# Optimization experiments

Measured on AMD Instinct MI355X. Metric: run time of the kernel, lower is better.

The kernel has to match this reference:

```python
import jax, jax.numpy as jnp
import numpy as np

P, NT = 4, 524288
DZ = 1.0e-3     # z step (m)
DT = 0.01       # time step (ps)
GAMMA = 1.0e-3  # nonlinear coefficient
FR = 0.18       # Raman fraction
OMEGA0 = 1830.0 # carrier angular frequency (rad/ps), ~1030 nm


def setup_inputs() -> dict:
    key = jax.random.key(0)
    ks = jax.random.split(key, 7)
    A_re = jax.random.normal(ks[0], (P, NT), jnp.float32) * 0.5
    A_im = jax.random.normal(ks[1], (P, NT), jnp.float32) * 0.5
    S = jax.random.uniform(ks[2], (P, P, P, P), jnp.float32) * 0.1  # mode overlap tensor
    D_re = jax.random.normal(ks[3], (P, NT), jnp.float32) * 0.1
    D_im = jax.random.normal(ks[4], (P, NT), jnp.float32) * 0.01
    hrw_re = jax.random.normal(ks[5], (NT,), jnp.float32)
    hrw_im = jax.random.normal(ks[6], (NT,), jnp.float32)
    omega = (2.0 * np.pi * np.fft.fftfreq(NT, DT)).astype(np.float32)
    return {"A_re": A_re, "A_im": A_im, "S": S, "D_re": D_re, "D_im": D_im,
            "hrw_re": hrw_re, "hrw_im": hrw_im, "omega": jnp.asarray(omega), "nz": 10}


def _propagate(A0, S, D, hrw, omega, nz):
    # half-step linear (dispersion) phase, applied in the frequency domain
    lin = jnp.exp(0.5j * DZ * D)                       # (P, Nt)
    # self-steepening spectral prefactor  i*gamma*(1 + Omega/omega0)
    pref = (1j * GAMMA) * (1.0 + omega / OMEGA0)       # (Nt,)
    hrw_c = jnp.conj(hrw)                              # (Nt,)

    def nl(A):  # dA/dz from Kerr + Raman + self-steepening, A: (P, Nt) time domain
        S_kerr = jnp.einsum('pqrs,qt,rt,st->pt', S, A, A, jnp.conj(A))
        T = A[:, None, :] * jnp.conj(A)[None, :, :]    # (P, P, Nt)
        T_conv = jnp.fft.ifft(jnp.fft.fft(T, axis=-1) * hrw_c, axis=-1) * DT
        Vpl = jnp.einsum('pmrs,rst->pmt', S, T_conv)   # (P, P, Nt)
        S_raman = jnp.einsum('pmt,mt->pt', Vpl, A)     # (P, Nt)
        S_total = (1.0 - FR) * S_kerr + FR * S_raman
        return jnp.fft.fft(pref * jnp.fft.ifft(S_total, axis=-1), axis=-1)

    def step(carry, _):
        f, fw = carry
        fw = fw * lin
        f = jnp.fft.fft(fw, axis=-1)
        # RK4 for the nonlinear sub-step
        k1 = DZ * nl(f)
        k2 = DZ * nl(f + 0.5 * k1)
        k3 = DZ * nl(f + 0.5 * k2)
        k4 = DZ * nl(f + k3)
        f = f + (k1 + 2.0 * k2 + 2.0 * k3 + k4) / 6.0
        fw = jnp.fft.ifft(f, axis=-1) * lin
        return (f, fw), None

    fw0 = jnp.fft.ifft(A0, axis=-1)
    (f, fw), _ = jax.lax.scan(step, (A0, fw0), None, length=nz)
    return jnp.fft.fft(fw, axis=-1)


def reference(A_re, A_im, S, D_re, D_im, hrw_re, hrw_im, omega, nz):
    A = (A_re + 1j * A_im).astype(jnp.complex64)
    D = (D_re + 1j * D_im).astype(jnp.complex64)
    hrw = (hrw_re + 1j * hrw_im).astype(jnp.complex64)
    out = _propagate(A, S, D, hrw, omega, nz)          # (P, Nt) complex64
    return jnp.stack([out.real, out.imag])             # (2, P, Nt) float32
```

## Files before the change

kernel.cpp:

```cpp
#include <hip/hip_runtime.h>
#include <math.h>

#define NTOT (1 << 19)
#define NN1 512
#define NN2 1024
#define PM 4
#define NZ_STEPS 10

static const float DZv = 1.0e-3f;
static const float DTv = 0.01f;
static const float GAMMAv = 1.0e-3f;
static const float FRv = 0.18f;
static const float OMEGA0v = 1830.0f;

typedef float2 cplx;
__device__ inline cplx cmul(cplx a, cplx b) { return make_float2(a.x * b.x - a.y * b.y, a.x * b.y + a.y * b.x); }
__device__ inline cplx cadd(cplx a, cplx b) { return make_float2(a.x + b.x, a.y + b.y); }
__device__ inline cplx csub(cplx a, cplx b) { return make_float2(a.x - b.x, a.y - b.y); }
__device__ inline cplx cscale(cplx a, float s) { return make_float2(a.x * s, a.y * s); }
__device__ inline cplx conjc(cplx a) { return make_float2(a.x, -a.y); }
__device__ inline cplx expi_pi(float a, float sgn) {
    float s, c;
    sincospif(a, &s, &c);
    return make_float2(c, sgn * s);
}
__device__ inline int dig4rev10(int j) {
    return ((j & 3) << 8) | (((j >> 2) & 3) << 6) | (((j >> 4) & 3) << 4) | (((j >> 6) & 3) << 2) | ((j >> 8) & 3);
}
__device__ inline int b4rev8(int t) {
    return ((t & 3) << 6) | (((t >> 2) & 3) << 4) | (((t >> 4) & 3) << 2) | ((t >> 6) & 3);
}
__device__ inline int islot_512(int k1) { return ((k1 & 1) << 8) | b4rev8(k1 >> 1); }

#define SK(q) ((q) + ((q) >> 4))

__device__ inline void wfence() {
    asm volatile("" ::: "memory");
    __builtin_amdgcn_wave_barrier();
    asm volatile("" ::: "memory");
}

#define TW_SZ 596
#define TWOFF(L) ((L) == 4 ? 0 : (L) == 16 ? 4 : (L) == 64 ? 20 : 84)
#define TWR2 340
__device__ inline void init_tw(cplx* tw, int tid) {
    for (int idx = tid; idx < TW_SZ; idx += 256) {
        float a;
        if (idx < 4) a = (float)idx * (0.5f / 4.0f);
        else if (idx < 20) a = (float)(idx - 4) * (0.5f / 16.0f);
        else if (idx < 84) a = (float)(idx - 20) * (0.5f / 64.0f);
        else if (idx < 340) a = (float)(idx - 84) * (0.5f / 256.0f);
        else a = (float)(idx - 340) * (1.0f / 256.0f);
        float s, c;
        sincospif(a, &s, &c);
        tw[idx] = make_float2(c, s);
    }
}
__device__ inline cplx twget(const cplx* tw, int off, int b, float SGN) {
    cplx t = tw[off + b];
    return make_float2(t.x, SGN * t.y);
}

__device__ inline void r4dif_w(cplx& x0, cplx& x1, cplx& x2, cplx& x3, cplx w1, float SGN) {
    cplx t0 = cadd(x0, x2), t1 = cadd(x1, x3), t2 = csub(x0, x2), t3 = csub(x1, x3);
    cplx ct3 = make_float2(-SGN * t3.y, SGN * t3.x);
    cplx w2 = cmul(w1, w1), w3 = cmul(w2, w1);
    x0 = cadd(t0, t1);
    x1 = cmul(cadd(t2, ct3), w1);
    x2 = cmul(csub(t0, t1), w2);
    x3 = cmul(csub(t2, ct3), w3);
}
__device__ inline void r4dif0(cplx& x0, cplx& x1, cplx& x2, cplx& x3, float SGN) {
    cplx t0 = cadd(x0, x2), t1 = cadd(x1, x3), t2 = csub(x0, x2), t3 = csub(x1, x3);
    cplx ct3 = make_float2(-SGN * t3.y, SGN * t3.x);
    x0 = cadd(t0, t1); x1 = cadd(t2, ct3); x2 = csub(t0, t1); x3 = csub(t2, ct3);
}
__device__ inline void r4dit_w(cplx& x0, cplx& x1, cplx& x2, cplx& x3, cplx w1, float SGN) {
    cplx w2 = cmul(w1, w1), w3 = cmul(w2, w1);
    cplx z1 = cmul(x1, w1), z2 = cmul(x2, w2), z3 = cmul(x3, w3);
    cplx t0 = cadd(x0, z2), t1 = cadd(z1, z3), t2 = csub(x0, z2), t3 = csub(z1, z3);
    cplx ct3 = make_float2(-SGN * t3.y, SGN * t3.x);
    x0 = cadd(t0, t1); x1 = cadd(t2, ct3); x2 = csub(t0, t1); x3 = csub(t2, ct3);
}
__device__ inline void r4dit0(cplx& x0, cplx& x1, cplx& x2, cplx& x3, float SGN) {
    cplx t0 = cadd(x0, x2), t1 = cadd(x1, x3), t2 = csub(x0, x2), t3 = csub(x1, x3);
    cplx ct3 = make_float2(-SGN * t3.y, SGN * t3.x);
    x0 = cadd(t0, t1); x1 = cadd(t2, ct3); x2 = csub(t0, t1); x3 = csub(t2, ct3);
}

template <int ISGN>
__device__ inline void fft_j2n2(const cplx* gsrc, cplx* y, cplx* ld, const cplx* tw, int tid) {
    const float SGN = (float)ISGN;
    const float4* s4 = (const float4*)gsrc;
    float4 va = s4[2 * tid], vb = s4[2 * tid + 1];
    cplx y0 = make_float2(va.x, va.y), y1 = make_float2(va.z, va.w);
    cplx y2 = make_float2(vb.x, vb.y), y3 = make_float2(vb.z, vb.w);
    r4dit0(y0, y1, y2, y3, SGN);
    int q0 = 4 * tid;
    ld[SK(q0)] = y0; ld[SK(q0 + 1)] = y1; ld[SK(q0 + 2)] = y2; ld[SK(q0 + 3)] = y3;
    wfence();
    #pragma unroll
    for (int L = 4; L <= 64; L <<= 2) {
        int b = tid & (L - 1), g = tid / L;
        int p0 = g * 4 * L + b;
        cplx z0 = ld[SK(p0)], z1 = ld[SK(p0 + L)], z2 = ld[SK(p0 + 2 * L)], z3 = ld[SK(p0 + 3 * L)];
        r4dit_w(z0, z1, z2, z3, twget(tw, TWOFF(L), b, SGN), SGN);
        ld[SK(p0)] = z0; ld[SK(p0 + L)] = z1; ld[SK(p0 + 2 * L)] = z2; ld[SK(p0 + 3 * L)] = z3;
        if (L == 64) __syncthreads();
        else wfence();
    }
    {
        int b = tid;
        cplx z0 = ld[SK(b)], z1 = ld[SK(b + 256)], z2 = ld[SK(b + 512)], z3 = ld[SK(b + 768)];
        r4dit_w(z0, z1, z2, z3, twget(tw, 84, b, SGN), SGN);
        y[0] = z0; y[1] = z1; y[2] = z2; y[3] = z3;
    }
}

template <bool INV>
__device__ inline void fft_n22j(cplx* y, cplx* ld, const cplx* tw, int tid, cplx w0, cplx dlt, cplx* gdst) {
    const float SGN = INV ? 1.0f : -1.0f;
    r4dif_w(y[0], y[1], y[2], y[3], twget(tw, 84, tid, SGN), SGN);
    ld[SK(tid)] = y[0]; ld[SK(tid + 256)] = y[1]; ld[SK(tid + 512)] = y[2]; ld[SK(tid + 768)] = y[3];
    __syncthreads();
    #pragma unroll
    for (int L = 64; L >= 4; L >>= 2) {
        int b = tid & (L - 1), g = tid / L;
        int p0 = g * 4 * L + b;
        cplx z0 = ld[SK(p0)], z1 = ld[SK(p0 + L)], z2 = ld[SK(p0 + 2 * L)], z3 = ld[SK(p0 + 3 * L)];
        r4dif_w(z0, z1, z2, z3, twget(tw, TWOFF(L), b, SGN), SGN);
        ld[SK(p0)] = z0; ld[SK(p0 + L)] = z1; ld[SK(p0 + 2 * L)] = z2; ld[SK(p0 + 3 * L)] = z3;
        wfence();
    }
    {
        int p0 = 4 * tid;
        cplx z0 = ld[SK(p0)], z1 = ld[SK(p0 + 1)], z2 = ld[SK(p0 + 2)], z3 = ld[SK(p0 + 3)];
        r4dif0(z0, z1, z2, z3, SGN);
        cplx w = INV ? cscale(w0, 1.0f / (float)NTOT) : w0;
        cplx o0 = cmul(z0, w); w = cmul(w, dlt);
        cplx o1 = cmul(z1, w); w = cmul(w, dlt);
        cplx o2 = cmul(z2, w); w = cmul(w, dlt);
        cplx o3 = cmul(z3, w);
        float4* d4 = (float4*)(gdst + p0);
        d4[0] = make_float4(o0.x, o0.y, o1.x, o1.y);
        d4[1] = make_float4(o2.x, o2.y, o3.x, o3.y);
    }
}

template <bool INV>
__global__ __launch_bounds__(256) void kA1(const cplx* __restrict__ in, cplx* __restrict__ out) {
    __shared__ cplx ld[1024 + 64];
    __shared__ cplx tw[TW_SZ];
    int row = blockIdx.y;
    int n1 = blockIdx.x;
    int tid = threadIdx.x;
    const cplx* src = in + (size_t)row * NTOT;
    cplx* dst = out + (size_t)row * NTOT;
    size_t base = (size_t)n1 * NN2;
    cplx y[4];
    y[0] = src[base + tid];
    y[1] = src[base + tid + 256];
    y[2] = src[base + tid + 512];
    y[3] = src[base + tid + 768];
    init_tw(tw, tid);
    __syncthreads();
    const float SGN = INV ? 1.0f : -1.0f;
    cplx w0 = expi_pi((float)(n1 * dig4rev10(4 * tid)) * (2.0f / (float)NTOT), SGN);
    cplx dlt = expi_pi((float)n1 * (1.0f / 1024.0f), SGN);
    fft_n22j<INV>(y, ld, tw, tid, w0, dlt, dst + base);
}

#define APPLY_CT(o, n1v)                                                        \
    {                                                                           \
        cplx W0 = expi_pi((float)((n1v) * k2b) * (2.0f / (float)NTOT), SGN_B);  \
        if (CONV) W0 = cscale(W0, 1.0f / (float)NTOT);                          \
        cplx P1 = expi_pi((float)(n1v) * (1.0f / 1024.0f), SGN_B);              \
        cplx P2 = expi_pi((float)(n1v) * (1.0f / 4096.0f), SGN_B);              \
        cplx wct = W0;                                                          \
        o[0] = cmul(o[0], wct);                                                 \
        wct = cmul(wct, P1); o[1] = cmul(o[1], wct);                            \
        wct = cmul(wct, P1); o[2] = cmul(o[2], wct);                            \
        wct = cmul(wct, P1); o[3] = cmul(o[3], wct);                            \
        wct = cmul(W0, P2);  o[4] = cmul(o[4], wct);                            \
        wct = cmul(wct, P1); o[5] = cmul(o[5], wct);                            \
        wct = cmul(wct, P1); o[6] = cmul(o[6], wct);                            \
        wct = cmul(wct, P1); o[7] = cmul(o[7], wct);                            \
    }

template <bool CONV, int TMODE>
__global__ __launch_bounds__(256) void kM(const cplx* in, cplx* out, const cplx* __restrict__ tab) {
    __shared__ cplx ld[8 * 545];
    __shared__ cplx tw[TW_SZ];
    const float SGN_F = CONV ? -1.0f : 1.0f;
    const float SGN_B = -SGN_F;
    int row = blockIdx.y;
    int jb = blockIdx.x * 8;
    const cplx* src = in + (size_t)row * NTOT;
    cplx* dst = out + (size_t)row * NTOT;
    const cplx* trow = (TMODE == 3) ? tab : tab + (size_t)row * NTOT;
    int tid = threadIdx.x;
    int jj = tid & 7, n10 = tid >> 3;
    cplx v[16];
    #pragma unroll
    for (int m = 0; m < 16; m++) v[m] = src[(size_t)(n10 + 32 * m) * NN2 + jb + jj];
    init_tw(tw, tid);
    __syncthreads();
    #pragma unroll
    for (int m = 0; m < 8; m++) {
        int b = n10 + 32 * m;
        cplx u = v[m], w = v[m + 8];
        v[m] = cadd(u, w);
        v[m + 8] = cmul(csub(u, w), twget(tw, TWR2, b, SGN_F));
    }
    #pragma unroll
    for (int m = 0; m < 8; m++) {
        int b = n10 + 32 * m;
        ld[jj * 545 + SK(b)] = v[m];
        ld[jj * 545 + SK(b + 256)] = v[m + 8];
    }
    __syncthreads();
    {
        int r = tid >> 5;
        cplx* rp = ld + r * 545;
        #pragma unroll
        for (int L = 64; L >= 4; L >>= 2) {
            #pragma unroll
            for (int it = 0; it < 4; it++) {
                int idx = (tid & 31) + 32 * it;
                int h = idx >> 6, s = idx & 63;
                int b = s & (L - 1), g = s / L;
                int q0 = h * 256 + g * 4 * L + b;
                cplx y0 = rp[SK(q0)], y1 = rp[SK(q0 + L)], y2 = rp[SK(q0 + 2 * L)], y3 = rp[SK(q0 + 3 * L)];
                r4dif_w(y0, y1, y2, y3, twget(tw, TWOFF(L), b, SGN_F), SGN_F);
                rp[SK(q0)] = y0; rp[SK(q0 + L)] = y1; rp[SK(q0 + 2 * L)] = y2; rp[SK(q0 + 3 * L)] = y3;
            }
            wfence();
        }
        #pragma unroll
        for (int it = 0; it < 4; it++) {
            int idx = (tid & 31) + 32 * it;
            int h = idx >> 6, s = idx & 63;
            int q0 = h * 256 + 4 * s;
            cplx y0 = rp[SK(q0)], y1 = rp[SK(q0 + 1)], y2 = rp[SK(q0 + 2)], y3 = rp[SK(q0 + 3)];
            r4dif0(y0, y1, y2, y3, SGN_F);
            size_t tb = (size_t)(jb + r) * NN1 + q0;
            const cplx* tp = trow + tb;
            cplx t0 = tp[0], t1 = tp[1], t2 = tp[2], t3 = tp[3];
            if (TMODE == 2) { t0 = cmul(t0, t0); t1 = cmul(t1, t1); t2 = cmul(t2, t2); t3 = cmul(t3, t3); }
            y0 = cmul(y0, t0); y1 = cmul(y1, t1); y2 = cmul(y2, t2); y3 = cmul(y3, t3);
            r4dit0(y0, y1, y2, y3, SGN_B);
            rp[SK(q0)] = y0; rp[SK(q0 + 1)] = y1; rp[SK(q0 + 2)] = y2; rp[SK(q0 + 3)] = y3;
        }
        wfence();
        #pragma unroll
        for (int L = 4; L <= 64; L <<= 2) {
            #pragma unroll
            for (int it = 0; it < 4; it++) {
                int idx = (tid & 31) + 32 * it;
                int h = idx >> 6, s = idx & 63;
                int b = s & (L - 1), g = s / L;
                int q0 = h * 256 + g * 4 * L + b;
                cplx y0 = rp[SK(q0)], y1 = rp[SK(q0 + L)], y2 = rp[SK(q0 + 2 * L)], y3 = rp[SK(q0 + 3 * L)];
                r4dit_w(y0, y1, y2, y3, twget(tw, TWOFF(L), b, SGN_B), SGN_B);
                rp[SK(q0)] = y0; rp[SK(q0 + L)] = y1; rp[SK(q0 + 2 * L)] = y2; rp[SK(q0 + 3 * L)] = y3;
            }
            wfence();
        }
    }
    __syncthreads();
    {
        int t = tid;
        cplx r2 = twget(tw, TWR2, t, SGN_B);
        cplx oa[8], ob[8];
        #pragma unroll
        for (int f = 0; f < 8; f++) {
            cplx u = ld[f * 545 + SK(t)];
            cplx w = ld[f * 545 + SK(t + 256)];
            cplx wv = cmul(w, r2);
            oa[f] = cadd(u, wv);
            ob[f] = csub(u, wv);
        }
        int k2b = dig4rev10(jb);
        APPLY_CT(oa, t);
        APPLY_CT(ob, t + 256);
        float4* da = (float4*)(dst + (size_t)t * NN2 + jb);
        da[0] = make_float4(oa[0].x, oa[0].y, oa[1].x, oa[1].y);
        da[1] = make_float4(oa[2].x, oa[2].y, oa[3].x, oa[3].y);
        da[2] = make_float4(oa[4].x, oa[4].y, oa[5].x, oa[5].y);
        da[3] = make_float4(oa[6].x, oa[6].y, oa[7].x, oa[7].y);
        float4* db = (float4*)(dst + (size_t)(t + 256) * NN2 + jb);
        db[0] = make_float4(ob[0].x, ob[0].y, ob[1].x, ob[1].y);
        db[1] = make_float4(ob[2].x, ob[2].y, ob[3].x, ob[3].y);
        db[2] = make_float4(ob[4].x, ob[4].y, ob[5].x, ob[5].y);
        db[3] = make_float4(ob[6].x, ob[6].y, ob[7].x, ob[7].y);
    }
}

__global__ __launch_bounds__(256) void kB2T(const cplx* __restrict__ in, cplx* __restrict__ out) {
    __shared__ cplx ld[1024 + 64];
    __shared__ cplx tw[TW_SZ];
    int row = blockIdx.y;
    int n1 = blockIdx.x;
    int tid = threadIdx.x;
    size_t base = (size_t)row * NTOT + (size_t)n1 * NN2;
    init_tw(tw, tid);
    __syncthreads();
    cplx y[4];
    fft_j2n2<-1>(in + base, y, ld, tw, tid);
    #pragma unroll
    for (int q = 0; q < 4; q++) out[base + tid + q * 256] = y[q];
}

__global__ __launch_bounds__(256) void kNL(const cplx* __restrict__ Zin, const cplx* __restrict__ A,
                                           const float* __restrict__ Sg, cplx* __restrict__ Tbout) {
    __shared__ cplx ld0[1024 + 64];
    __shared__ cplx ld1[1024 + 64];
    __shared__ cplx tw[TW_SZ];
    __shared__ float Ssh[256];
    int n1 = blockIdx.x, tid = threadIdx.x;
    Ssh[tid] = Sg[tid];
    init_tw(tw, tid);
    size_t base = (size_t)n1 * NN2;
    size_t tb = base + tid;
    cplx am[4][4];
    #pragma unroll
    for (int m = 0; m < 4; m++)
        #pragma unroll
        for (int q = 0; q < 4; q++) am[m][q] = A[(size_t)m * NTOT + tb + q * 256];
    cplx acc[4][4];
    #pragma unroll
    for (int p = 0; p < 4; p++)
        #pragma unroll
        for (int q = 0; q < 4; q++) acc[p][q] = make_float2(0.f, 0.f);
    __syncthreads();
    for (int rowi = 0; rowi < 16; rowi++) {
        cplx* buf = (rowi & 1) ? ld1 : ld0;
        cplx tc[4];
        fft_j2n2<1>(Zin + (size_t)rowi * NTOT + base, tc, buf, tw, tid);
        int r = rowi >> 2, s = rowi & 3;
        #pragma unroll
        for (int q = 0; q < 4; q++) {
            #pragma unroll
            for (int p = 0; p < 4; p++) {
                float c0 = Ssh[((p * 4 + 0) * 4 + r) * 4 + s];
                float c1 = Ssh[((p * 4 + 1) * 4 + r) * 4 + s];
                float c2 = Ssh[((p * 4 + 2) * 4 + r) * 4 + s];
                float c3 = Ssh[((p * 4 + 3) * 4 + r) * 4 + s];
                cplx c;
                c.x = c0 * am[0][q].x + c1 * am[1][q].x + c2 * am[2][q].x + c3 * am[3][q].x;
                c.y = c0 * am[0][q].y + c1 * am[1][q].y + c2 * am[2][q].y + c3 * am[3][q].y;
                acc[p][q] = cadd(acc[p][q], cmul(c, tc[q]));
            }
        }
    }
    #pragma unroll
    for (int q = 0; q < 4; q++) {
        cplx pp[4][4];
        #pragma unroll
        for (int r = 0; r < 4; r++)
            #pragma unroll
            for (int s = 0; s < 4; s++) pp[r][s] = cmul(am[r][q], conjc(am[s][q]));
        #pragma unroll
        for (int p = 0; p < 4; p++) {
            cplx kc = make_float2(0.f, 0.f);
            #pragma unroll
            for (int m = 0; m < 4; m++) {
                cplx g = make_float2(0.f, 0.f);
                #pragma unroll
                for (int r = 0; r < 4; r++)
                    #pragma unroll
                    for (int s = 0; s < 4; s++) {
                        float coef = Ssh[((p * 4 + m) * 4 + r) * 4 + s];
                        g.x += coef * pp[r][s].x;
                        g.y += coef * pp[r][s].y;
                    }
                kc = cadd(kc, cmul(g, am[m][q]));
            }
            acc[p][q] = cadd(cscale(kc, 1.0f - FRv), cscale(acc[p][q], FRv));
        }
    }
    cplx w0 = expi_pi((float)(n1 * dig4rev10(4 * tid)) * (2.0f / (float)NTOT), 1.0f);
    cplx dlt = expi_pi((float)n1 * (1.0f / 1024.0f), 1.0f);
    #pragma unroll
    for (int p = 0; p < 4; p++) {
        cplx* buf = (p & 1) ? ld1 : ld0;
        cplx y[4] = {acc[p][0], acc[p][1], acc[p][2], acc[p][3]};
        fft_n22j<true>(y, buf, tw, tid, w0, dlt, Tbout + (size_t)p * NTOT + base);
    }
}

template <int STAGE>
__global__ __launch_bounds__(256) void kRK(const cplx* Tbin, const cplx* __restrict__ fP,
                                           cplx* __restrict__ kaccP, cplx* __restrict__ AtmpP,
                                           cplx* ZOut) {
    __shared__ cplx ld0[1024 + 64];
    __shared__ cplx ld1[1024 + 64];
    __shared__ cplx tw[TW_SZ];
    int n1 = blockIdx.x, tid = threadIdx.x;
    init_tw(tw, tid);
    __syncthreads();
    size_t base = (size_t)n1 * NN2;
    cplx an[4][4];
    #pragma unroll
    for (int p = 0; p < 4; p++) {
        cplx* buf = (p & 1) ? ld1 : ld0;
        cplx y[4];
        fft_j2n2<-1>(Tbin + (size_t)p * NTOT + base, y, buf, tw, tid);
        #pragma unroll
        for (int q = 0; q < 4; q++) {
            size_t off = (size_t)p * NTOT + base + tid + q * 256;
            cplx v = y[q];
            if (STAGE == 1) {
                kaccP[off] = v;
                an[p][q] = cadd(fP[off], cscale(v, 0.5f));
                AtmpP[off] = an[p][q];
            } else if (STAGE == 2) {
                kaccP[off] = cadd(kaccP[off], cscale(v, 2.0f));
                an[p][q] = cadd(fP[off], cscale(v, 0.5f));
                AtmpP[off] = an[p][q];
            } else if (STAGE == 3) {
                kaccP[off] = cadd(kaccP[off], cscale(v, 2.0f));
                an[p][q] = cadd(fP[off], v);
                AtmpP[off] = an[p][q];
            } else {
                an[p][q] = cadd(fP[off], cscale(cadd(kaccP[off], v), 1.0f / 6.0f));
            }
        }
    }
    const float SGN = (STAGE == 4) ? 1.0f : -1.0f;
    cplx w0 = expi_pi((float)(n1 * dig4rev10(4 * tid)) * (2.0f / (float)NTOT), SGN);
    cplx dlt = expi_pi((float)n1 * (1.0f / 1024.0f), SGN);
    if (STAGE <= 3) {
        #pragma unroll
        for (int rs = 0; rs < 16; rs++) {
            cplx* buf = (rs & 1) ? ld1 : ld0;
            int r = rs >> 2, s = rs & 3;
            cplx y[4];
            #pragma unroll
            for (int q = 0; q < 4; q++) y[q] = cmul(an[r][q], conjc(an[s][q]));
            fft_n22j<false>(y, buf, tw, tid, w0, dlt, ZOut + (size_t)rs * NTOT + base);
        }
    } else {
        #pragma unroll
        for (int p = 0; p < 4; p++) {
            cplx* buf = (p & 1) ? ld1 : ld0;
            cplx y[4] = {an[p][0], an[p][1], an[p][2], an[p][3]};
            fft_n22j<true>(y, buf, tw, tid, w0, dlt, ZOut + (size_t)p * NTOT + base);
        }
    }
}

__global__ __launch_bounds__(256) void kBD(const cplx* __restrict__ Tbin, cplx* __restrict__ fP,
                                           cplx* __restrict__ ZOut) {
    __shared__ cplx ld0[1024 + 64];
    __shared__ cplx ld1[1024 + 64];
    __shared__ cplx tw[TW_SZ];
    int n1 = blockIdx.x, tid = threadIdx.x;
    init_tw(tw, tid);
    __syncthreads();
    size_t base = (size_t)n1 * NN2;
    cplx an[4][4];
    #pragma unroll
    for (int p = 0; p < 4; p++) {
        cplx* buf = (p & 1) ? ld1 : ld0;
        cplx y[4];
        fft_j2n2<-1>(Tbin + (size_t)p * NTOT + base, y, buf, tw, tid);
        #pragma unroll
        for (int q = 0; q < 4; q++) {
            size_t off = (size_t)p * NTOT + base + tid + q * 256;
            an[p][q] = y[q];
            fP[off] = y[q];
        }
    }
    cplx w0 = expi_pi((float)(n1 * dig4rev10(4 * tid)) * (2.0f / (float)NTOT), -1.0f);
    cplx dlt = expi_pi((float)n1 * (1.0f / 1024.0f), -1.0f);
    #pragma unroll
    for (int rs = 0; rs < 16; rs++) {
        cplx* buf = (rs & 1) ? ld1 : ld0;
        int r = rs >> 2, s = rs & 3;
        cplx y[4];
        #pragma unroll
        for (int q = 0; q < 4; q++) y[q] = cmul(an[r][q], conjc(an[s][q]));
        fft_n22j<false>(y, buf, tw, tid, w0, dlt, ZOut + (size_t)rs * NTOT + base);
    }
}

__global__ __launch_bounds__(256) void k_tables(const float* __restrict__ D_re, const float* __restrict__ D_im,
                                                const float* __restrict__ hrw_re, const float* __restrict__ hrw_im,
                                                const float* __restrict__ omega,
                                                cplx* __restrict__ lin, cplx* __restrict__ pref, cplx* __restrict__ hrwc) {
    int k = blockIdx.x * 256 + threadIdx.x;
    if (k >= NTOT) return;
    int k2 = k & (NN2 - 1), k1 = k >> 10;
    int j = dig4rev10(k2), i = islot_512(k1);
    int s2 = j * NN1 + i;
    float om = omega[k];
    pref[s2] = make_float2(0.0f, GAMMAv * DZv * (1.0f + om / OMEGA0v));
    hrwc[s2] = make_float2(hrw_re[k] * DTv, -hrw_im[k] * DTv);
    for (int p = 0; p < PM; p++) {
        float dr = D_re[(size_t)p * NTOT + k], di = D_im[(size_t)p * NTOT + k];
        float amp = expf(-0.5f * DZv * di);
        float s, c;
        sincosf(0.5f * DZv * dr, &s, &c);
        lin[(size_t)p * NTOT + s2] = make_float2(amp * c, amp * s);
    }
}

__global__ void k_in(const float* __restrict__ Are, const float* __restrict__ Aim, cplx* __restrict__ f) {
    __shared__ cplx t[32][33];
    int p = blockIdx.z;
    int n1b = blockIdx.x * 32, n2b = blockIdx.y * 32;
    int tx = threadIdx.x, ty = threadIdx.y;
    const float* ar = Are + (size_t)p * NTOT;
    const float* ai = Aim + (size_t)p * NTOT;
    for (int yy = ty; yy < 32; yy += 8) {
        size_t idx = (size_t)(n2b + yy) * NN1 + (n1b + tx);
        t[yy][tx] = make_float2(ar[idx], ai[idx]);
    }
    __syncthreads();
    cplx* dst = f + (size_t)p * NTOT;
    for (int yy = ty; yy < 32; yy += 8) {
        dst[(size_t)(n1b + yy) * NN2 + (n2b + tx)] = t[tx][yy];
    }
}

__global__ void k_out(const cplx* __restrict__ fin, float* __restrict__ out) {
    __shared__ cplx t[32][33];
    int p = blockIdx.z;
    int n1b = blockIdx.x * 32, n2b = blockIdx.y * 32;
    int tx = threadIdx.x, ty = threadIdx.y;
    const cplx* src = fin + (size_t)p * NTOT;
    for (int yy = ty; yy < 32; yy += 8) {
        t[yy][tx] = src[(size_t)(n1b + yy) * NN2 + (n2b + tx)];
    }
    __syncthreads();
    float* outr = out + (size_t)p * NTOT;
    float* outi = out + (size_t)(PM + p) * NTOT;
    for (int yy = ty; yy < 32; yy += 8) {
        cplx v = t[tx][yy];
        size_t idx = (size_t)(n2b + yy) * NN1 + (n1b + tx);
        outr[idx] = v.x;
        outi[idx] = v.y;
    }
}

extern "C" void kernel_launch(void* const* d_in, const int* in_sizes, int n_in,
                              void* d_out, int out_size, void* d_ws, size_t ws_size,
                              hipStream_t stream) {
    const float* Are = (const float*)d_in[0];
    const float* Aim = (const float*)d_in[1];
    const float* S = (const float*)d_in[2];
    const float* Dre = (const float*)d_in[3];
    const float* Dim = (const float*)d_in[4];
    const float* hre = (const float*)d_in[5];
    const float* him = (const float*)d_in[6];
    const float* omega = (const float*)d_in[7];

    const size_t ROW = (size_t)NTOT;
    if (ws_size < 38ULL * ROW * sizeof(cplx)) return;
    cplx* f = (cplx*)d_ws;
    cplx* Atmp = f + 4 * ROW;
    cplx* kacc = Atmp + 4 * ROW;
    cplx* lin = kacc + 4 * ROW;
    cplx* pref = lin + 4 * ROW;
    cplx* hrwc = pref + 1 * ROW;
    cplx* Tb = hrwc + 1 * ROW;
    cplx* Z = Tb + 4 * ROW;

    dim3 b256(256);
    dim3 gT(16, 32, 4), bT(32, 8);
    dim3 gPW1(NTOT / 256);

    k_tables<<<gPW1, b256, 0, stream>>>(Dre, Dim, hre, him, omega, lin, pref, hrwc);
    k_in<<<gT, bT, 0, stream>>>(Are, Aim, f);
    kA1<true><<<dim3(512, 4), b256, 0, stream>>>(f, Tb);

    for (int step = 0; step < NZ_STEPS; step++) {
        if (step == 0)
            kM<false, 1><<<dim3(128, 4), b256, 0, stream>>>(Tb, Tb, lin);
        else
            kM<false, 2><<<dim3(128, 4), b256, 0, stream>>>(Tb, Tb, lin);
        kBD<<<dim3(512), b256, 0, stream>>>(Tb, f, Z);
        for (int st = 1; st <= 4; st++) {
            const cplx* Aarg = (st == 1) ? f : Atmp;
            kM<true, 3><<<dim3(128, 16), b256, 0, stream>>>(Z, Z, hrwc);
            kNL<<<dim3(512), b256, 0, stream>>>(Z, Aarg, S, Tb);
            kM<false, 3><<<dim3(128, 4), b256, 0, stream>>>(Tb, Tb, pref);
            if (st == 1)
                kRK<1><<<dim3(512), b256, 0, stream>>>(Tb, f, kacc, Atmp, Z);
            else if (st == 2)
                kRK<2><<<dim3(512), b256, 0, stream>>>(Tb, f, kacc, Atmp, Z);
            else if (st == 3)
                kRK<3><<<dim3(512), b256, 0, stream>>>(Tb, f, kacc, Atmp, Z);
            else
                kRK<4><<<dim3(512), b256, 0, stream>>>(Tb, f, kacc, nullptr, Tb);
        }
    }
    kM<false, 1><<<dim3(128, 4), b256, 0, stream>>>(Tb, Tb, lin);
    kB2T<<<dim3(512, 4), b256, 0, stream>>>(Tb, Atmp);
    k_out<<<gT, bT, 0, stream>>>(Atmp, (float*)d_out);
}
```

Baseline: 8.299 ms.

## Exploit Hermitian symmetry of Raman outer-product to transform only 10 of 16 rows

The outer-product tensor T[r,s]=A_r*conj(A_s) is Hermitian, so only the 10 upper-triangle rows are formed and forward-FFTed. The convolution kernel kMC derives the lower-triangle rows from them with a reversed, conjugated Raman table (gtab), writing rows 10-15. kNL then remaps row indices and conjugates where needed. This cuts the FFT and memory traffic in the producer kernels, at the cost of one extra table and a second pass inside the off-diagonal convolution blocks.

```diff
diff --git a/kernel.cpp b/kernel.cpp
--- a/kernel.cpp
+++ b/kernel.cpp
@@ -209,14 +209,8 @@
     for (int m = 0; m < 8; m++) {
         int b = n10 + 32 * m;
         cplx u = v[m], w = v[m + 8];
-        v[m] = cadd(u, w);
-        v[m + 8] = cmul(csub(u, w), twget(tw, TWR2, b, SGN_F));
-    }
-    #pragma unroll
-    for (int m = 0; m < 8; m++) {
-        int b = n10 + 32 * m;
-        ld[jj * 545 + SK(b)] = v[m];
-        ld[jj * 545 + SK(b + 256)] = v[m + 8];
+        ld[jj * 545 + SK(b)] = cadd(u, w);
+        ld[jj * 545 + SK(b + 256)] = cmul(csub(u, w), twget(tw, TWR2, b, SGN_F));
     }
     __syncthreads();
     {
@@ -296,6 +290,112 @@
     }
 }
 
+__global__ __launch_bounds__(256) void kMC(const cplx* in, cplx* out,
+                                           const cplx* __restrict__ tabW, const cplx* __restrict__ tabU) {
+    __shared__ cplx ld[8 * 545];
+    __shared__ cplx tw[TW_SZ];
+    constexpr bool CONV = true;
+    const float SGN_F = -1.0f, SGN_B = 1.0f;
+    int oy = blockIdx.y;
+    int jb = blockIdx.x * 8;
+    const cplx* src = in + (size_t)oy * NTOT;
+    int tid = threadIdx.x;
+    int jj = tid & 7, n10 = tid >> 3;
+    cplx v[16];
+    #pragma unroll
+    for (int m = 0; m < 16; m++) v[m] = src[(size_t)(n10 + 32 * m) * NN2 + jb + jj];
+    init_tw(tw, tid);
+    __syncthreads();
+    int npass = (oy < 4) ? 1 : 2;
+    for (int pass = 0; pass < npass; pass++) {
+        const cplx* trow = (npass == 2 && pass == 0) ? tabU : tabW;
+        int orow = (npass == 2 && pass == 0) ? (10 + oy - 4) : oy;
+        cplx* dst = out + (size_t)orow * NTOT;
+        if (pass == 1) __syncthreads();
+        #pragma unroll
+        for (int m = 0; m < 8; m++) {
+            int b = n10 + 32 * m;
+            cplx u = v[m], w = v[m + 8];
+            ld[jj * 545 + SK(b)] = cadd(u, w);
+            ld[jj * 545 + SK(b + 256)] = cmul(csub(u, w), twget(tw, TWR2, b, SGN_F));
+        }
+        __syncthreads();
+        {
+            int r = tid >> 5;
+            cplx* rp = ld + r * 545;
+            #pragma unroll
+            for (int L = 64; L >= 4; L >>= 2) {
+                #pragma unroll
+                for (int it = 0; it < 4; it++) {
+                    int idx = (tid & 31) + 32 * it;
+                    int h = idx >> 6, s = idx & 63;
+                    int b = s & (L - 1), g = s / L;
+                    int q0 = h * 256 + g * 4 * L + b;
+                    cplx y0 = rp[SK(q0)], y1 = rp[SK(q0 + L)], y2 = rp[SK(q0 + 2 * L)], y3 = rp[SK(q0 + 3 * L)];
+                    r4dif_w(y0, y1, y2, y3, twget(tw, TWOFF(L), b, SGN_F), SGN_F);
+                    rp[SK(q0)] = y0; rp[SK(q0 + L)] = y1; rp[SK(q0 + 2 * L)] = y2; rp[SK(q0 + 3 * L)] = y3;
+                }
+                wfence();
+            }
+            #pragma unroll
+            for (int it = 0; it < 4; it++) {
+                int idx = (tid & 31) + 32 * it;
+                int h = idx >> 6, s = idx & 63;
+                int q0 = h * 256 + 4 * s;
+                cplx y0 = rp[SK(q0)], y1 = rp[SK(q0 + 1)], y2 = rp[SK(q0 + 2)], y3 = rp[SK(q0 + 3)];
+                r4dif0(y0, y1, y2, y3, SGN_F);
+                size_t tb = (size_t)(jb + r) * NN1 + q0;
+                const cplx* tp = trow + tb;
+                y0 = cmul(y0, tp[0]); y1 = cmul(y1, tp[1]); y2 = cmul(y2, tp[2]); y3 = cmul(y3, tp[3]);
+                r4dit0(y0, y1, y2, y3, SGN_B);
+                rp[SK(q0)] = y0; rp[SK(q0 + 1)] = y1; rp[SK(q0 + 2)] = y2; rp[SK(q0 + 3)] = y3;
+            }
+            wfence();
+            #pragma unroll
+            for (int L = 4; L <= 64; L <<= 2) {
+                #pragma unroll
+                for (int it = 0; it < 4; it++) {
+                    int idx = (tid & 31) + 32 * it;
+                    int h = idx >> 6, s = idx & 63;
+                    int b = s & (L - 1), g = s / L;
+                    int q0 = h * 256 + g * 4 * L + b;
+                    cplx y0 = rp[SK(q0)], y1 = rp[SK(q0 + L)], y2 = rp[SK(q0 + 2 * L)], y3 = rp[SK(q0 + 3 * L)];
+                    r4dit_w(y0, y1, y2, y3, twget(tw, TWOFF(L), b, SGN_B), SGN_B);
+                    rp[SK(q0)] = y0; rp[SK(q0 + L)] = y1; rp[SK(q0 + 2 * L)] = y2; rp[SK(q0 + 3 * L)] = y3;
+                }
+                wfence();
+            }
+        }
+        __syncthreads();
+        {
+            int t = tid;
+            cplx r2 = twget(tw, TWR2, t, SGN_B);
+            cplx oa[8], ob[8];
+            #pragma unroll
+            for (int f = 0; f < 8; f++) {
+                cplx u = ld[f * 545 + SK(t)];
+                cplx w = ld[f * 545 + SK(t + 256)];
+                cplx wv = cmul(w, r2);
+                oa[f] = cadd(u, wv);
+                ob[f] = csub(u, wv);
+            }
+            int k2b = dig4rev10(jb);
+            APPLY_CT(oa, t);
+            APPLY_CT(ob, t + 256);
+            float4* da = (float4*)(dst + (size_t)t * NN2 + jb);
+            da[0] = make_float4(oa[0].x, oa[0].y, oa[1].x, oa[1].y);
+            da[1] = make_float4(oa[2].x, oa[2].y, oa[3].x, oa[3].y);
+            da[2] = make_float4(oa[4].x, oa[4].y, oa[5].x, oa[5].y);
+            da[3] = make_float4(oa[6].x, oa[6].y, oa[7].x, oa[7].y);
+            float4* db = (float4*)(dst + (size_t)(t + 256) * NN2 + jb);
+            db[0] = make_float4(ob[0].x, ob[0].y, ob[1].x, ob[1].y);
+            db[1] = make_float4(ob[2].x, ob[2].y, ob[3].x, ob[3].y);
+            db[2] = make_float4(ob[4].x, ob[4].y, ob[5].x, ob[5].y);
+            db[3] = make_float4(ob[6].x, ob[6].y, ob[7].x, ob[7].y);
+        }
+    }
+}
+
 __global__ __launch_bounds__(256) void kB2T(const cplx* __restrict__ in, cplx* __restrict__ out) {
     __shared__ cplx ld[1024 + 64];
     __shared__ cplx tw[TW_SZ];
@@ -333,13 +433,22 @@
         #pragma unroll
         for (int q = 0; q < 4; q++) acc[p][q] = make_float2(0.f, 0.f);
     __syncthreads();
+    const unsigned RP = (0u << 0) | (1u << 2) | (2u << 4) | (3u << 6) | (0u << 8) | (0u << 10) | (0u << 12) |
+                        (1u << 14) | (1u << 16) | (2u << 18) | (1u << 20) | (2u << 22) | (3u << 24) |
+                        (2u << 26) | (3u << 28) | (3u << 30);
+    const unsigned SP = (0u << 0) | (1u << 2) | (2u << 4) | (3u << 6) | (1u << 8) | (2u << 10) | (3u << 12) |
+                        (2u << 14) | (3u << 16) | (3u << 18) | (0u << 20) | (0u << 22) | (0u << 24) |
+                        (1u << 26) | (1u << 28) | (2u << 30);
     for (int rowi = 0; rowi < 16; rowi++) {
         cplx* buf = (rowi & 1) ? ld1 : ld0;
         cplx tc[4];
         fft_j2n2<1>(Zin + (size_t)rowi * NTOT + base, tc, buf, tw, tid);
-        int r = rowi >> 2, s = rowi & 3;
+        int r = (int)((RP >> (2 * rowi)) & 3u);
+        int s = (int)((SP >> (2 * rowi)) & 3u);
+        float csg = (rowi >= 10) ? -1.0f : 1.0f;
         #pragma unroll
         for (int q = 0; q < 4; q++) {
+            cplx tcq = make_float2(tc[q].x, csg * tc[q].y);
             #pragma unroll
             for (int p = 0; p < 4; p++) {
                 float c0 = Ssh[((p * 4 + 0) * 4 + r) * 4 + s];
@@ -349,7 +458,7 @@
                 cplx c;
                 c.x = c0 * am[0][q].x + c1 * am[1][q].x + c2 * am[2][q].x + c3 * am[3][q].x;
                 c.y = c0 * am[0][q].y + c1 * am[1][q].y + c2 * am[2][q].y + c3 * am[3][q].y;
-                acc[p][q] = cadd(acc[p][q], cmul(c, tc[q]));
+                acc[p][q] = cadd(acc[p][q], cmul(c, tcq));
             }
         }
     }
@@ -431,14 +540,16 @@
     cplx w0 = expi_pi((float)(n1 * dig4rev10(4 * tid)) * (2.0f / (float)NTOT), SGN);
     cplx dlt = expi_pi((float)n1 * (1.0f / 1024.0f), SGN);
     if (STAGE <= 3) {
-        #pragma unroll
-        for (int rs = 0; rs < 16; rs++) {
-            cplx* buf = (rs & 1) ? ld1 : ld0;
-            int r = rs >> 2, s = rs & 3;
+        const int R10[10] = {0, 1, 2, 3, 0, 0, 0, 1, 1, 2};
+        const int S10[10] = {0, 1, 2, 3, 1, 2, 3, 2, 3, 3};
+        #pragma unroll
+        for (int rw = 0; rw < 10; rw++) {
+            cplx* buf = (rw & 1) ? ld1 : ld0;
+            int r = R10[rw], s = S10[rw];
             cplx y[4];
             #pragma unroll
             for (int q = 0; q < 4; q++) y[q] = cmul(an[r][q], conjc(an[s][q]));
-            fft_n22j<false>(y, buf, tw, tid, w0, dlt, ZOut + (size_t)rs * NTOT + base);
+            fft_n22j<false>(y, buf, tw, tid, w0, dlt, ZOut + (size_t)rw * NTOT + base);
         }
     } else {
         #pragma unroll
@@ -474,21 +585,24 @@
     }
     cplx w0 = expi_pi((float)(n1 * dig4rev10(4 * tid)) * (2.0f / (float)NTOT), -1.0f);
     cplx dlt = expi_pi((float)n1 * (1.0f / 1024.0f), -1.0f);
-    #pragma unroll
-    for (int rs = 0; rs < 16; rs++) {
-        cplx* buf = (rs & 1) ? ld1 : ld0;
-        int r = rs >> 2, s = rs & 3;
+    const int R10[10] = {0, 1, 2, 3, 0, 0, 0, 1, 1, 2};
+    const int S10[10] = {0, 1, 2, 3, 1, 2, 3, 2, 3, 3};
+    #pragma unroll
+    for (int rw = 0; rw < 10; rw++) {
+        cplx* buf = (rw & 1) ? ld1 : ld0;
+        int r = R10[rw], s = S10[rw];
         cplx y[4];
         #pragma unroll
         for (int q = 0; q < 4; q++) y[q] = cmul(an[r][q], conjc(an[s][q]));
-        fft_n22j<false>(y, buf, tw, tid, w0, dlt, ZOut + (size_t)rs * NTOT + base);
+        fft_n22j<false>(y, buf, tw, tid, w0, dlt, ZOut + (size_t)rw * NTOT + base);
     }
 }
 
 __global__ __launch_bounds__(256) void k_tables(const float* __restrict__ D_re, const float* __restrict__ D_im,
                                                 const float* __restrict__ hrw_re, const float* __restrict__ hrw_im,
                                                 const float* __restrict__ omega,
-                                                cplx* __restrict__ lin, cplx* __restrict__ pref, cplx* __restrict__ hrwc) {
+                                                cplx* __restrict__ lin, cplx* __restrict__ pref,
+                                                cplx* __restrict__ hrwc, cplx* __restrict__ gtab) {
     int k = blockIdx.x * 256 + threadIdx.x;
     if (k >= NTOT) return;
     int k2 = k & (NN2 - 1), k1 = k >> 10;
@@ -497,6 +611,8 @@
     float om = omega[k];
     pref[s2] = make_float2(0.0f, GAMMAv * DZv * (1.0f + om / OMEGA0v));
     hrwc[s2] = make_float2(hrw_re[k] * DTv, -hrw_im[k] * DTv);
+    int kr = (NTOT - k) & (NTOT - 1);
+    gtab[s2] = make_float2(hrw_re[kr] * DTv, hrw_im[kr] * DTv);
     for (int p = 0; p < PM; p++) {
         float dr = D_re[(size_t)p * NTOT + k], di = D_im[(size_t)p * NTOT + k];
         float amp = expf(-0.5f * DZv * di);
@@ -557,21 +673,22 @@
     const float* omega = (const float*)d_in[7];
 
     const size_t ROW = (size_t)NTOT;
-    if (ws_size < 38ULL * ROW * sizeof(cplx)) return;
+    if (ws_size < 39ULL * ROW * sizeof(cplx)) return;
     cplx* f = (cplx*)d_ws;
     cplx* Atmp = f + 4 * ROW;
     cplx* kacc = Atmp + 4 * ROW;
     cplx* lin = kacc + 4 * ROW;
     cplx* pref = lin + 4 * ROW;
     cplx* hrwc = pref + 1 * ROW;
-    cplx* Tb = hrwc + 1 * ROW;
+    cplx* gtab = hrwc + 1 * ROW;
+    cplx* Tb = gtab + 1 * ROW;
     cplx* Z = Tb + 4 * ROW;
 
     dim3 b256(256);
     dim3 gT(16, 32, 4), bT(32, 8);
     dim3 gPW1(NTOT / 256);
 
-    k_tables<<<gPW1, b256, 0, stream>>>(Dre, Dim, hre, him, omega, lin, pref, hrwc);
+    k_tables<<<gPW1, b256, 0, stream>>>(Dre, Dim, hre, him, omega, lin, pref, hrwc, gtab);
     k_in<<<gT, bT, 0, stream>>>(Are, Aim, f);
     kA1<true><<<dim3(512, 4), b256, 0, stream>>>(f, Tb);
 
@@ -583,7 +700,7 @@
         kBD<<<dim3(512), b256, 0, stream>>>(Tb, f, Z);
         for (int st = 1; st <= 4; st++) {
             const cplx* Aarg = (st == 1) ? f : Atmp;
-            kM<true, 3><<<dim3(128, 16), b256, 0, stream>>>(Z, Z, hrwc);
+            kMC<<<dim3(128, 10), b256, 0, stream>>>(Z, Z, hrwc, gtab);
             kNL<<<dim3(512), b256, 0, stream>>>(Z, Aarg, S, Tb);
             kM<false, 3><<<dim3(128, 4), b256, 0, stream>>>(Tb, Tb, pref);
             if (st == 1)
```

Result: no change. 8.354 ms (+0.7%).

## Exploit Hermitian symmetry of outer products to skip six Raman FFT rows

Applied to the files above, without the earlier changes.

The Raman outer product T[r,s] = A_r conj(A_s) is Hermitian in (r,s), so only the 10 upper-triangle rows are forward-transformed. The 6 lower rows are rebuilt in the convolution pass from the upper rows' spectra, using a frequency-reversed hrw table written to spare rows. The nonlinear kernel reads them back with conjugation via packed r/s index maps. This cuts forward FFT work and memory traffic for the 16 T rows, at the cost of an extra table, an extra launch and more index logic. A small butterfly store fusion is also included.

```diff
diff --git a/kernel.cpp b/kernel.cpp
--- a/kernel.cpp
+++ b/kernel.cpp
@@ -209,14 +209,8 @@
     for (int m = 0; m < 8; m++) {
         int b = n10 + 32 * m;
         cplx u = v[m], w = v[m + 8];
-        v[m] = cadd(u, w);
-        v[m + 8] = cmul(csub(u, w), twget(tw, TWR2, b, SGN_F));
-    }
-    #pragma unroll
-    for (int m = 0; m < 8; m++) {
-        int b = n10 + 32 * m;
-        ld[jj * 545 + SK(b)] = v[m];
-        ld[jj * 545 + SK(b + 256)] = v[m + 8];
+        ld[jj * 545 + SK(b)] = cadd(u, w);
+        ld[jj * 545 + SK(b + 256)] = cmul(csub(u, w), twget(tw, TWR2, b, SGN_F));
     }
     __syncthreads();
     {
@@ -333,13 +327,22 @@
         #pragma unroll
         for (int q = 0; q < 4; q++) acc[p][q] = make_float2(0.f, 0.f);
     __syncthreads();
+    const unsigned RP = (0u << 0) | (1u << 2) | (2u << 4) | (3u << 6) | (0u << 8) | (0u << 10) | (0u << 12) |
+                        (1u << 14) | (1u << 16) | (2u << 18) | (1u << 20) | (2u << 22) | (3u << 24) |
+                        (2u << 26) | (3u << 28) | (3u << 30);
+    const unsigned SP = (0u << 0) | (1u << 2) | (2u << 4) | (3u << 6) | (1u << 8) | (2u << 10) | (3u << 12) |
+                        (2u << 14) | (3u << 16) | (3u << 18) | (0u << 20) | (0u << 22) | (0u << 24) |
+                        (1u << 26) | (1u << 28) | (2u << 30);
     for (int rowi = 0; rowi < 16; rowi++) {
         cplx* buf = (rowi & 1) ? ld1 : ld0;
         cplx tc[4];
         fft_j2n2<1>(Zin + (size_t)rowi * NTOT + base, tc, buf, tw, tid);
-        int r = rowi >> 2, s = rowi & 3;
+        int r = (int)((RP >> (2 * rowi)) & 3u);
+        int s = (int)((SP >> (2 * rowi)) & 3u);
+        float csg = (rowi >= 10) ? -1.0f : 1.0f;
         #pragma unroll
         for (int q = 0; q < 4; q++) {
+            cplx tcq = make_float2(tc[q].x, csg * tc[q].y);
             #pragma unroll
             for (int p = 0; p < 4; p++) {
                 float c0 = Ssh[((p * 4 + 0) * 4 + r) * 4 + s];
@@ -349,7 +352,7 @@
                 cplx c;
                 c.x = c0 * am[0][q].x + c1 * am[1][q].x + c2 * am[2][q].x + c3 * am[3][q].x;
                 c.y = c0 * am[0][q].y + c1 * am[1][q].y + c2 * am[2][q].y + c3 * am[3][q].y;
-                acc[p][q] = cadd(acc[p][q], cmul(c, tc[q]));
+                acc[p][q] = cadd(acc[p][q], cmul(c, tcq));
             }
         }
     }
@@ -431,14 +434,16 @@
     cplx w0 = expi_pi((float)(n1 * dig4rev10(4 * tid)) * (2.0f / (float)NTOT), SGN);
     cplx dlt = expi_pi((float)n1 * (1.0f / 1024.0f), SGN);
     if (STAGE <= 3) {
-        #pragma unroll
-        for (int rs = 0; rs < 16; rs++) {
-            cplx* buf = (rs & 1) ? ld1 : ld0;
-            int r = rs >> 2, s = rs & 3;
+        const int R10[10] = {0, 1, 2, 3, 0, 0, 0, 1, 1, 2};
+        const int S10[10] = {0, 1, 2, 3, 1, 2, 3, 2, 3, 3};
+        #pragma unroll
+        for (int rw = 0; rw < 10; rw++) {
+            cplx* buf = (rw & 1) ? ld1 : ld0;
+            int r = R10[rw], s = S10[rw];
             cplx y[4];
             #pragma unroll
             for (int q = 0; q < 4; q++) y[q] = cmul(an[r][q], conjc(an[s][q]));
-            fft_n22j<false>(y, buf, tw, tid, w0, dlt, ZOut + (size_t)rs * NTOT + base);
+            fft_n22j<false>(y, buf, tw, tid, w0, dlt, ZOut + (size_t)rw * NTOT + base);
         }
     } else {
         #pragma unroll
@@ -474,21 +479,24 @@
     }
     cplx w0 = expi_pi((float)(n1 * dig4rev10(4 * tid)) * (2.0f / (float)NTOT), -1.0f);
     cplx dlt = expi_pi((float)n1 * (1.0f / 1024.0f), -1.0f);
-    #pragma unroll
-    for (int rs = 0; rs < 16; rs++) {
-        cplx* buf = (rs & 1) ? ld1 : ld0;
-        int r = rs >> 2, s = rs & 3;
+    const int R10[10] = {0, 1, 2, 3, 0, 0, 0, 1, 1, 2};
+    const int S10[10] = {0, 1, 2, 3, 1, 2, 3, 2, 3, 3};
+    #pragma unroll
+    for (int rw = 0; rw < 10; rw++) {
+        cplx* buf = (rw & 1) ? ld1 : ld0;
+        int r = R10[rw], s = S10[rw];
         cplx y[4];
         #pragma unroll
         for (int q = 0; q < 4; q++) y[q] = cmul(an[r][q], conjc(an[s][q]));
-        fft_n22j<false>(y, buf, tw, tid, w0, dlt, ZOut + (size_t)rs * NTOT + base);
+        fft_n22j<false>(y, buf, tw, tid, w0, dlt, ZOut + (size_t)rw * NTOT + base);
     }
 }
 
 __global__ __launch_bounds__(256) void k_tables(const float* __restrict__ D_re, const float* __restrict__ D_im,
                                                 const float* __restrict__ hrw_re, const float* __restrict__ hrw_im,
                                                 const float* __restrict__ omega,
-                                                cplx* __restrict__ lin, cplx* __restrict__ pref, cplx* __restrict__ hrwc) {
+                                                cplx* __restrict__ lin, cplx* __restrict__ pref,
+                                                cplx* __restrict__ hrwc, cplx* __restrict__ gtab) {
     int k = blockIdx.x * 256 + threadIdx.x;
     if (k >= NTOT) return;
     int k2 = k & (NN2 - 1), k1 = k >> 10;
@@ -497,6 +505,8 @@
     float om = omega[k];
     pref[s2] = make_float2(0.0f, GAMMAv * DZv * (1.0f + om / OMEGA0v));
     hrwc[s2] = make_float2(hrw_re[k] * DTv, -hrw_im[k] * DTv);
+    int kr = (NTOT - k) & (NTOT - 1);
+    gtab[s2] = make_float2(hrw_re[kr] * DTv, hrw_im[kr] * DTv);
     for (int p = 0; p < PM; p++) {
         float dr = D_re[(size_t)p * NTOT + k], di = D_im[(size_t)p * NTOT + k];
         float amp = expf(-0.5f * DZv * di);
@@ -557,21 +567,22 @@
     const float* omega = (const float*)d_in[7];
 
     const size_t ROW = (size_t)NTOT;
-    if (ws_size < 38ULL * ROW * sizeof(cplx)) return;
+    if (ws_size < 39ULL * ROW * sizeof(cplx)) return;
     cplx* f = (cplx*)d_ws;
     cplx* Atmp = f + 4 * ROW;
     cplx* kacc = Atmp + 4 * ROW;
     cplx* lin = kacc + 4 * ROW;
     cplx* pref = lin + 4 * ROW;
     cplx* hrwc = pref + 1 * ROW;
-    cplx* Tb = hrwc + 1 * ROW;
+    cplx* gtab = hrwc + 1 * ROW;
+    cplx* Tb = gtab + 1 * ROW;
     cplx* Z = Tb + 4 * ROW;
 
     dim3 b256(256);
     dim3 gT(16, 32, 4), bT(32, 8);
     dim3 gPW1(NTOT / 256);
 
-    k_tables<<<gPW1, b256, 0, stream>>>(Dre, Dim, hre, him, omega, lin, pref, hrwc);
+    k_tables<<<gPW1, b256, 0, stream>>>(Dre, Dim, hre, him, omega, lin, pref, hrwc, gtab);
     k_in<<<gT, bT, 0, stream>>>(Are, Aim, f);
     kA1<true><<<dim3(512, 4), b256, 0, stream>>>(f, Tb);
 
@@ -583,7 +594,8 @@
         kBD<<<dim3(512), b256, 0, stream>>>(Tb, f, Z);
         for (int st = 1; st <= 4; st++) {
             const cplx* Aarg = (st == 1) ? f : Atmp;
-            kM<true, 3><<<dim3(128, 16), b256, 0, stream>>>(Z, Z, hrwc);
+            kM<true, 3><<<dim3(128, 6), b256, 0, stream>>>(Z + 4 * ROW, Z + 10 * ROW, gtab);
+            kM<true, 3><<<dim3(128, 10), b256, 0, stream>>>(Z, Z, hrwc);
             kNL<<<dim3(512), b256, 0, stream>>>(Z, Aarg, S, Tb);
             kM<false, 3><<<dim3(128, 4), b256, 0, stream>>>(Tb, Tb, pref);
             if (st == 1)
```

After: 8.402 ms. Within noise of the previous version (+1.2%).
